# Kernel optimization log

Hardware: AMD Instinct MI355X
Metric: run time of the kernel (lower is better)

Reference implementation:

```python
import jax, jax.numpy as jnp
import numpy as np

HC = 4           # hc_mult
ITERS = 20       # hc_sinkhorn_iters
EPS = 1e-6       # hc_eps
NORM_EPS = 1e-6  # rms_norm_eps


def setup_inputs() -> dict:
    key = jax.random.key(0)
    k = jax.random.split(key, 4)
    B, S, H = 1, 4096, 4096
    mix = (2 + HC) * HC  # 24
    hidden_states = jax.random.normal(k[0], (B, S, HC, H), jnp.float32)
    hc_fn = jax.random.normal(k[1], (mix, HC * H), jnp.float32) * 0.02
    hc_base = jax.random.normal(k[2], (mix,), jnp.float32) * 0.02
    hc_scale = jnp.ones((3,), jnp.float32)
    norm_weight = jnp.ones((H,), jnp.float32)
    w_inner = jax.random.normal(k[3], (H, H), jnp.float32) * 0.02
    return {
        "hidden_states": hidden_states,
        "hc_fn": hc_fn,
        "hc_base": hc_base,
        "hc_scale": hc_scale,
        "norm_weight": norm_weight,
        "w_inner": w_inner,
    }


def reference(hidden_states, hc_fn, hc_base, hc_scale, norm_weight, w_inner):
    B, S, hc, H = hidden_states.shape
    # RMS stat over the flattened (hc*H) feature dim
    flat = hidden_states.reshape(B, S, hc * H).astype(jnp.float32)
    rs = jax.lax.rsqrt(jnp.mean(jnp.square(flat), axis=-1, keepdims=True) + NORM_EPS)
    mixes = jnp.einsum('bsd,md->bsm', flat, hc_fn) * rs  # [B,S,(2+hc)*hc]

    ps, qs, cs = hc_scale[0], hc_scale[1], hc_scale[2]
    pre = jax.nn.sigmoid(mixes[..., :hc] * ps + hc_base[:hc]) + EPS           # [B,S,hc]
    post = jax.nn.sigmoid(mixes[..., hc:2 * hc] * qs + hc_base[hc:2 * hc]) + EPS
    comb = jax.nn.sigmoid(
        mixes[..., 2 * hc:].reshape(B, S, hc, hc) * cs
        + hc_base[2 * hc:].reshape(hc, hc)
    ) + EPS  # [B,S,hc,hc]

    # 20-iter Sinkhorn row/column normalization
    def sink(_, c):
        c = c / (jnp.sum(c, axis=-1, keepdims=True) + EPS)
        return c / (jnp.sum(c, axis=-2, keepdims=True) + EPS)
    comb = jax.lax.fori_loop(0, ITERS, sink, comb)

    # weighted stream reduction -> [B,S,H]
    reduced = jnp.einsum('bsh,bshd->bsd', pre, hidden_states)

    # norm + inner sub-block (RMSNorm then dense projection)
    nr = jax.lax.rsqrt(jnp.mean(jnp.square(reduced), axis=-1, keepdims=True) + NORM_EPS)
    normed = reduced * nr * norm_weight
    out = jnp.einsum('bsd,ed->bse', normed, w_inner)  # [B,S,H]

    # broadcast back to streams: post-gated write + Sinkhorn-mixed residual
    expanded = post[..., None] * out[:, :, None, :] \
        + jnp.einsum('bshk,bskd->bshd', comb, hidden_states)
    return expanded.astype(hidden_states.dtype)
```

## Files before the change

kernel.cpp:

```cpp
#include <hip/hip_runtime.h>
#include <math.h>

#define S_DIM 4096
#define H_DIM 4096
#define HC_N 4
#define HD_DIM 16384
#define MIXN 24
#define SINK_IT 20

typedef float f32x4 __attribute__((ext_vector_type(4)));
typedef __bf16 bf16x8 __attribute__((ext_vector_type(8)));
typedef unsigned short u16x8 __attribute__((ext_vector_type(8)));
typedef unsigned short u16x4 __attribute__((ext_vector_type(4)));

__device__ __forceinline__ unsigned short f2bf(float f) {
  unsigned u = __builtin_bit_cast(unsigned, f);
  u += 0x7FFFu + ((u >> 16) & 1u);
  return (unsigned short)(u >> 16);
}
__device__ __forceinline__ float bf2f(unsigned short h) {
  return __builtin_bit_cast(float, (unsigned)h << 16);
}

__global__ __launch_bounds__(256) void k_w2bf(const float* __restrict__ w,
                                              unsigned short* __restrict__ wb) {
  const size_t i = (size_t)(blockIdx.x * 256 + threadIdx.x) * 8;
  f32x4 a = *(const f32x4*)(w + i);
  f32x4 b = *(const f32x4*)(w + i + 4);
  u16x8 o;
  o[0] = f2bf(a.x); o[1] = f2bf(a.y); o[2] = f2bf(a.z); o[3] = f2bf(a.w);
  o[4] = f2bf(b.x); o[5] = f2bf(b.y); o[6] = f2bf(b.z); o[7] = f2bf(b.w);
  *(u16x8*)(wb + i) = o;
}

__global__ __launch_bounds__(256) void k_mixes(const float* __restrict__ hs,
                                               const float* __restrict__ fn,
                                               float* __restrict__ mixraw,
                                               float* __restrict__ sumsq) {
  __shared__ __align__(16) float lds[HC_N][1024];
  const int tid = threadIdx.x;
  const int b = blockIdx.x;
  const int lane = tid & 63, wave = tid >> 6;
  const int mbase = wave * 6;

  float acc[HC_N][6];
  float ss[HC_N];
#pragma unroll
  for (int r = 0; r < HC_N; r++) {
    ss[r] = 0.f;
#pragma unroll
    for (int j = 0; j < 6; j++) acc[r][j] = 0.f;
  }

  const size_t rowbase = (size_t)b * HC_N * HD_DIM;
  for (int it = 0; it < 16; ++it) {
    __syncthreads();
#pragma unroll
    for (int r = 0; r < HC_N; r++) {
      f32x4 v = *(const f32x4*)(hs + rowbase + (size_t)r * HD_DIM + it * 1024 + tid * 4);
      *(f32x4*)(&lds[r][tid * 4]) = v;
    }
    __syncthreads();
#pragma unroll
    for (int ii = 0; ii < 4; ii++) {
      const int c4 = ii * 64 + lane;
      f32x4 h4[HC_N];
#pragma unroll
      for (int r = 0; r < HC_N; r++) h4[r] = *(const f32x4*)(&lds[r][c4 * 4]);
      if (wave == 0) {
#pragma unroll
        for (int r = 0; r < HC_N; r++)
          ss[r] += h4[r].x * h4[r].x + h4[r].y * h4[r].y + h4[r].z * h4[r].z + h4[r].w * h4[r].w;
      }
#pragma unroll
      for (int j = 0; j < 6; j++) {
        f32x4 fv = *(const f32x4*)(fn + (size_t)(mbase + j) * HD_DIM + it * 1024 + c4 * 4);
#pragma unroll
        for (int r = 0; r < HC_N; r++)
          acc[r][j] += h4[r].x * fv.x + h4[r].y * fv.y + h4[r].z * fv.z + h4[r].w * fv.w;
      }
    }
  }

#pragma unroll
  for (int r = 0; r < HC_N; r++) {
#pragma unroll
    for (int j = 0; j < 6; j++) {
      float v = acc[r][j];
#pragma unroll
      for (int off = 32; off >= 1; off >>= 1) v += __shfl_xor(v, off, 64);
      if (lane == 0) mixraw[(size_t)(b * 4 + r) * MIXN + mbase + j] = v;
    }
  }
  if (wave == 0) {
#pragma unroll
    for (int r = 0; r < HC_N; r++) {
      float v = ss[r];
#pragma unroll
      for (int off = 32; off >= 1; off >>= 1) v += __shfl_xor(v, off, 64);
      if (lane == 0) sumsq[b * 4 + r] = v;
    }
  }
}

__global__ __launch_bounds__(256) void k_gates(const float* __restrict__ mixraw,
                                               const float* __restrict__ sumsq,
                                               const float* __restrict__ hbase,
                                               const float* __restrict__ hscale,
                                               float* __restrict__ gates) {
  const int row = blockIdx.x * 256 + threadIdx.x;
  const float rs = rsqrtf(sumsq[row] * (1.0f / HD_DIM) + 1e-6f);
  const float ps = hscale[0], qs = hscale[1], cs = hscale[2];
  const float* mr = mixraw + (size_t)row * MIXN;
  float g[MIXN];
#pragma unroll
  for (int m = 0; m < MIXN; m++) {
    const float sc = (m < 4) ? ps : ((m < 8) ? qs : cs);
    const float x = mr[m] * rs * sc + hbase[m];
    g[m] = 1.0f / (1.0f + expf(-x)) + 1e-6f;
  }
  for (int t = 0; t < SINK_IT; t++) {
#pragma unroll
    for (int i = 0; i < 4; i++) {
      const float s = g[8 + i * 4 + 0] + g[8 + i * 4 + 1] + g[8 + i * 4 + 2] + g[8 + i * 4 + 3] + 1e-6f;
#pragma unroll
      for (int j = 0; j < 4; j++) g[8 + i * 4 + j] /= s;
    }
#pragma unroll
    for (int j = 0; j < 4; j++) {
      const float s = g[8 + 0 + j] + g[8 + 4 + j] + g[8 + 8 + j] + g[8 + 12 + j] + 1e-6f;
#pragma unroll
      for (int i = 0; i < 4; i++) g[8 + i * 4 + j] /= s;
    }
  }
  float* go = gates + (size_t)row * MIXN;
#pragma unroll
  for (int m = 0; m < MIXN; m++) go[m] = g[m];
}

__global__ __launch_bounds__(256) void k_reduce_norm(const float* __restrict__ hs,
                                                     const float* __restrict__ gates,
                                                     const float* __restrict__ nw,
                                                     unsigned short* __restrict__ normed) {
  const int s = blockIdx.x, tid = threadIdx.x;
  const int lane = tid & 63, wave = tid >> 6;
  const float* g = gates + (size_t)s * MIXN;
  const float p0 = g[0], p1 = g[1], p2 = g[2], p3 = g[3];
  const size_t base = (size_t)s * HC_N * H_DIM;

  f32x4 red[4];
  float ssq = 0.f;
#pragma unroll
  for (int it = 0; it < 4; ++it) {
    const int d4 = it * 256 + tid;
    f32x4 a = *(const f32x4*)(hs + base + (size_t)0 * H_DIM + (size_t)d4 * 4);
    f32x4 b = *(const f32x4*)(hs + base + (size_t)1 * H_DIM + (size_t)d4 * 4);
    f32x4 c = *(const f32x4*)(hs + base + (size_t)2 * H_DIM + (size_t)d4 * 4);
    f32x4 d = *(const f32x4*)(hs + base + (size_t)3 * H_DIM + (size_t)d4 * 4);
    f32x4 v = p0 * a + p1 * b + p2 * c + p3 * d;
    red[it] = v;
    ssq += v.x * v.x + v.y * v.y + v.z * v.z + v.w * v.w;
  }
#pragma unroll
  for (int off = 32; off >= 1; off >>= 1) ssq += __shfl_xor(ssq, off, 64);
  __shared__ float ls[4];
  if (lane == 0) ls[wave] = ssq;
  __syncthreads();
  const float tot = ls[0] + ls[1] + ls[2] + ls[3];
  const float nr = rsqrtf(tot * (1.0f / H_DIM) + 1e-6f);
#pragma unroll
  for (int it = 0; it < 4; ++it) {
    const int d4 = it * 256 + tid;
    f32x4 w = *(const f32x4*)(nw + (size_t)d4 * 4);
    f32x4 v = red[it] * nr;
    v = v * w;
    u16x4 o;
    o[0] = f2bf(v.x); o[1] = f2bf(v.y); o[2] = f2bf(v.z); o[3] = f2bf(v.w);
    *(u16x4*)(normed + (size_t)s * H_DIM + (size_t)d4 * 4) = o;
  }
}

__device__ __forceinline__ void gload_lds16(const unsigned short* g, unsigned short* l) {
  __builtin_amdgcn_global_load_lds(
      (const __attribute__((address_space(1))) unsigned int*)(const void*)g,
      (__attribute__((address_space(3))) unsigned int*)(void*)l, 16, 0, 0);
}

#define VMW(n) asm volatile("s_waitcnt vmcnt(" #n ")" ::: "memory")
#define BAR    asm volatile("s_barrier" ::: "memory")
#define LGK0   asm volatile("s_waitcnt lgkmcnt(0)" ::: "memory")
#define SCB    __builtin_amdgcn_sched_barrier(0)

__global__ __launch_bounds__(512, 2) void k_gemm(const unsigned short* __restrict__ A,
                                                 const unsigned short* __restrict__ B,
                                                 unsigned short* __restrict__ C) {
  __shared__ __align__(16) unsigned short sAbuf[2][2][256 * 32];
  __shared__ __align__(16) unsigned short sBbuf[2][2][256 * 32];
  const int tid = threadIdx.x;
  const int lane = tid & 63, wave = tid >> 6;

  const int bid = blockIdx.x;
  const int v = bid & 7, u = bid >> 3;
  const int bm = u & 15, bn = v * 2 + (u >> 4);
  const int wm = wave >> 2, wn = wave & 3;

  const int srow = lane >> 2;
  const int sk8 = (((lane & 3) ^ ((lane >> 3) & 3)) * 8);
  const unsigned short* gA = A + (size_t)(bm * 256 + wave * 32 + srow) * 4096 + sk8;
  const unsigned short* gB = B + (size_t)(bn * 256 + wave * 32 + srow) * 4096 + sk8;
  const int ld0 = wave * 1024 + lane * 8;
  const int ld1 = ld0 + 512;

  f32x4 acc[8][4];
  f32x4 zero = {0.f, 0.f, 0.f, 0.f};
#pragma unroll
  for (int mf = 0; mf < 8; mf++)
#pragma unroll
    for (int nf = 0; nf < 4; nf++) acc[mf][nf] = zero;
  bf16x8 af[8];

  const int frow = lane & 15;
  const int fk = (((lane >> 4) ^ ((lane >> 1) & 3)) * 8);

#define PHASE_BODY(db, kh, nh, dostg, sdst, gsrc, t, skh) do {                  \
    if ((nh) == 0) {                                                            \
      _Pragma("unroll") for (int mf = 0; mf < 8; mf++)                          \
        af[mf] = *(const bf16x8*)&sAbuf[db][kh][(wm * 128 + mf * 16 + frow) * 32 + fk]; \
    }                                                                           \
    bf16x8 b0 = *(const bf16x8*)&sBbuf[db][kh][(wn * 64 + ((nh) * 2 + 0) * 16 + frow) * 32 + fk]; \
    bf16x8 b1 = *(const bf16x8*)&sBbuf[db][kh][(wn * 64 + ((nh) * 2 + 1) * 16 + frow) * 32 + fk]; \
    if (dostg) {                                                                \
      const unsigned short* _g = (gsrc) + (size_t)(t) * 64 + (skh) * 32;        \
      gload_lds16(_g,              (sdst) + ld0);                               \
      gload_lds16(_g + 16 * 4096,  (sdst) + ld1);                               \
    }                                                                           \
    SCB;                                                                        \
    BAR;                                                                        \
    LGK0;                                                                       \
    SCB;                                                                        \
    __builtin_amdgcn_s_setprio(1);                                              \
    _Pragma("unroll") for (int mf = 0; mf < 8; mf++) {                          \
      acc[mf][(nh) * 2 + 0] = __builtin_amdgcn_mfma_f32_16x16x32_bf16(af[mf], b0, acc[mf][(nh) * 2 + 0], 0, 0, 0); \
      acc[mf][(nh) * 2 + 1] = __builtin_amdgcn_mfma_f32_16x16x32_bf16(af[mf], b1, acc[mf][(nh) * 2 + 1], 0, 0, 0); \
    }                                                                           \
    __builtin_amdgcn_s_setprio(0);                                              \
    SCB;                                                                        \
  } while (0)

  gload_lds16(gA,                  &sAbuf[0][0][0] + ld0);
  gload_lds16(gA + 16 * 4096,      &sAbuf[0][0][0] + ld1);
  gload_lds16(gB,                  &sBbuf[0][0][0] + ld0);
  gload_lds16(gB + 16 * 4096,      &sBbuf[0][0][0] + ld1);
  gload_lds16(gA + 32,             &sAbuf[0][1][0] + ld0);
  gload_lds16(gA + 32 + 16 * 4096, &sAbuf[0][1][0] + ld1);
  gload_lds16(gB + 32,             &sBbuf[0][1][0] + ld0);
  gload_lds16(gB + 32 + 16 * 4096, &sBbuf[0][1][0] + ld1);
  VMW(4);
  BAR;

  for (int i = 0; i < 31; ++i) {
    const int t1 = 2 * i + 1, t2 = 2 * i + 2;
    PHASE_BODY(0, 0, 0, 1, &sAbuf[1][0][0], gA, t1, 0);          BAR;
    PHASE_BODY(0, 0, 1, 1, &sBbuf[1][0][0], gB, t1, 0); VMW(4);  BAR;
    PHASE_BODY(0, 1, 0, 1, &sAbuf[1][1][0], gA, t1, 1);          BAR;
    PHASE_BODY(0, 1, 1, 1, &sBbuf[1][1][0], gB, t1, 1); VMW(4);  BAR;
    PHASE_BODY(1, 0, 0, 1, &sAbuf[0][0][0], gA, t2, 0);          BAR;
    PHASE_BODY(1, 0, 1, 1, &sBbuf[0][0][0], gB, t2, 0); VMW(4);  BAR;
    PHASE_BODY(1, 1, 0, 1, &sAbuf[0][1][0], gA, t2, 1);          BAR;
    PHASE_BODY(1, 1, 1, 1, &sBbuf[0][1][0], gB, t2, 1); VMW(4);  BAR;
  }
  PHASE_BODY(0, 0, 0, 1, &sAbuf[1][0][0], gA, 63, 0);            BAR;
  PHASE_BODY(0, 0, 1, 1, &sBbuf[1][0][0], gB, 63, 0); VMW(4);    BAR;
  PHASE_BODY(0, 1, 0, 1, &sAbuf[1][1][0], gA, 63, 1);            BAR;
  PHASE_BODY(0, 1, 1, 1, &sBbuf[1][1][0], gB, 63, 1); VMW(0);    BAR;
  PHASE_BODY(1, 0, 0, 0, &sAbuf[0][0][0], gA, 0, 0);             BAR;
  PHASE_BODY(1, 0, 1, 0, &sAbuf[0][0][0], gA, 0, 0);             BAR;
  PHASE_BODY(1, 1, 0, 0, &sAbuf[0][0][0], gA, 0, 0);             BAR;
  PHASE_BODY(1, 1, 1, 0, &sAbuf[0][0][0], gA, 0, 0);

#undef PHASE_BODY

  const int crow0 = bm * 256 + wm * 128 + (lane >> 4) * 4;
  const int ccol0 = bn * 256 + wn * 64 + (lane & 15);
#pragma unroll
  for (int mf = 0; mf < 8; mf++)
#pragma unroll
    for (int nf = 0; nf < 4; nf++)
#pragma unroll
      for (int j = 0; j < 4; j++)
        C[(size_t)(crow0 + mf * 16 + j) * 4096 + ccol0 + nf * 16] = f2bf(acc[mf][nf][j]);
}

__global__ __launch_bounds__(256) void k_expand(const float* __restrict__ hs,
                                                const unsigned short* __restrict__ outb,
                                                const float* __restrict__ gates,
                                                float* __restrict__ y) {
  const int s = blockIdx.x, tid = threadIdx.x;
  const float* g = gates + (size_t)s * MIXN;
  float post[4], cb[4][4];
#pragma unroll
  for (int h = 0; h < 4; h++) post[h] = g[4 + h];
#pragma unroll
  for (int h = 0; h < 4; h++)
#pragma unroll
    for (int k = 0; k < 4; k++) cb[h][k] = g[8 + h * 4 + k];

  const size_t base = (size_t)s * HC_N * H_DIM;
#pragma unroll
  for (int it = 0; it < 4; ++it) {
    const int d4 = it * 256 + tid;
    f32x4 hv[4];
#pragma unroll
    for (int k = 0; k < 4; k++)
      hv[k] = *(const f32x4*)(hs + base + (size_t)k * H_DIM + (size_t)d4 * 4);
    u16x4 ob = *(const u16x4*)(outb + (size_t)s * H_DIM + (size_t)d4 * 4);
    f32x4 o = {bf2f(ob[0]), bf2f(ob[1]), bf2f(ob[2]), bf2f(ob[3])};
#pragma unroll
    for (int h = 0; h < 4; h++) {
      f32x4 e = post[h] * o + cb[h][0] * hv[0] + cb[h][1] * hv[1] + cb[h][2] * hv[2] + cb[h][3] * hv[3];
      *(f32x4*)(y + base + (size_t)h * H_DIM + (size_t)d4 * 4) = e;
    }
  }
}

extern "C" void kernel_launch(void* const* d_in, const int* in_sizes, int n_in,
                              void* d_out, int out_size, void* d_ws, size_t ws_size,
                              hipStream_t stream) {
  const float* hs = (const float*)d_in[0];
  const float* fn = (const float*)d_in[1];
  const float* hbase = (const float*)d_in[2];
  const float* hscale = (const float*)d_in[3];
  const float* nw = (const float*)d_in[4];
  const float* wi = (const float*)d_in[5];
  float* y = (float*)d_out;

  char* ws = (char*)d_ws;
  float* mixraw = (float*)(ws);
  float* sumsq = (float*)(ws + 393216);
  float* gates = (float*)(ws + 409600);
  unsigned short* normed = (unsigned short*)(ws + 1048576);
  unsigned short* wb = (unsigned short*)(ws + 1048576 + 33554432);
  unsigned short* outb = (unsigned short*)(ws + 1048576 + 2 * 33554432);

  k_w2bf<<<8192, 256, 0, stream>>>(wi, wb);
  k_mixes<<<1024, 256, 0, stream>>>(hs, fn, mixraw, sumsq);
  k_gates<<<16, 256, 0, stream>>>(mixraw, sumsq, hbase, hscale, gates);
  k_reduce_norm<<<4096, 256, 0, stream>>>(hs, gates, nw, normed);
  k_gemm<<<256, 512, 0, stream>>>(normed, wb, outb);
  k_expand<<<4096, 256, 0, stream>>>(hs, outb, gates, y);
}
```

Baseline: 484.3 us.

## Fuse gate/Sinkhorn computation into mixes kernel and register-prefetch inputs

Merges the separate gates kernel into the mixes kernel, so per-row mix results and sum-of-squares stay in shared memory and the gates are written directly. The mixes loop drops the LDS staging and block barriers: each wave now loads hidden-state and hc_fn vectors straight from global memory, with a one-iteration register prefetch. This removes one launch and the round trip of the intermediate buffers. The cost is that all four waves now read the same hidden-state data redundantly from global memory or cache, and the Sinkhorn tail runs on only four threads per block.

```diff
diff --git a/kernel.cpp b/kernel.cpp
--- a/kernel.cpp
+++ b/kernel.cpp
@@ -35,107 +35,110 @@
 
 __global__ __launch_bounds__(256) void k_mixes(const float* __restrict__ hs,
                                                const float* __restrict__ fn,
-                                               float* __restrict__ mixraw,
-                                               float* __restrict__ sumsq) {
-  __shared__ __align__(16) float lds[HC_N][1024];
-  const int tid = threadIdx.x;
-  const int b = blockIdx.x;
-  const int lane = tid & 63, wave = tid >> 6;
-  const int mbase = wave * 6;
-
-  float acc[HC_N][6];
-  float ss[HC_N];
-#pragma unroll
-  for (int r = 0; r < HC_N; r++) {
-    ss[r] = 0.f;
-#pragma unroll
-    for (int j = 0; j < 6; j++) acc[r][j] = 0.f;
-  }
-
-  const size_t rowbase = (size_t)b * HC_N * HD_DIM;
-  for (int it = 0; it < 16; ++it) {
-    __syncthreads();
-#pragma unroll
-    for (int r = 0; r < HC_N; r++) {
-      f32x4 v = *(const f32x4*)(hs + rowbase + (size_t)r * HD_DIM + it * 1024 + tid * 4);
-      *(f32x4*)(&lds[r][tid * 4]) = v;
-    }
-    __syncthreads();
-#pragma unroll
-    for (int ii = 0; ii < 4; ii++) {
-      const int c4 = ii * 64 + lane;
-      f32x4 h4[HC_N];
-#pragma unroll
-      for (int r = 0; r < HC_N; r++) h4[r] = *(const f32x4*)(&lds[r][c4 * 4]);
-      if (wave == 0) {
-#pragma unroll
-        for (int r = 0; r < HC_N; r++)
-          ss[r] += h4[r].x * h4[r].x + h4[r].y * h4[r].y + h4[r].z * h4[r].z + h4[r].w * h4[r].w;
-      }
-#pragma unroll
-      for (int j = 0; j < 6; j++) {
-        f32x4 fv = *(const f32x4*)(fn + (size_t)(mbase + j) * HD_DIM + it * 1024 + c4 * 4);
-#pragma unroll
-        for (int r = 0; r < HC_N; r++)
-          acc[r][j] += h4[r].x * fv.x + h4[r].y * fv.y + h4[r].z * fv.z + h4[r].w * fv.w;
-      }
-    }
-  }
-
-#pragma unroll
-  for (int r = 0; r < HC_N; r++) {
-#pragma unroll
-    for (int j = 0; j < 6; j++) {
-      float v = acc[r][j];
-#pragma unroll
-      for (int off = 32; off >= 1; off >>= 1) v += __shfl_xor(v, off, 64);
-      if (lane == 0) mixraw[(size_t)(b * 4 + r) * MIXN + mbase + j] = v;
-    }
-  }
-  if (wave == 0) {
-#pragma unroll
-    for (int r = 0; r < HC_N; r++) {
-      float v = ss[r];
-#pragma unroll
-      for (int off = 32; off >= 1; off >>= 1) v += __shfl_xor(v, off, 64);
-      if (lane == 0) sumsq[b * 4 + r] = v;
-    }
-  }
-}
-
-__global__ __launch_bounds__(256) void k_gates(const float* __restrict__ mixraw,
-                                               const float* __restrict__ sumsq,
                                                const float* __restrict__ hbase,
                                                const float* __restrict__ hscale,
                                                float* __restrict__ gates) {
-  const int row = blockIdx.x * 256 + threadIdx.x;
-  const float rs = rsqrtf(sumsq[row] * (1.0f / HD_DIM) + 1e-6f);
-  const float ps = hscale[0], qs = hscale[1], cs = hscale[2];
-  const float* mr = mixraw + (size_t)row * MIXN;
-  float g[MIXN];
-#pragma unroll
-  for (int m = 0; m < MIXN; m++) {
-    const float sc = (m < 4) ? ps : ((m < 8) ? qs : cs);
-    const float x = mr[m] * rs * sc + hbase[m];
-    g[m] = 1.0f / (1.0f + expf(-x)) + 1e-6f;
-  }
-  for (int t = 0; t < SINK_IT; t++) {
-#pragma unroll
-    for (int i = 0; i < 4; i++) {
-      const float s = g[8 + i * 4 + 0] + g[8 + i * 4 + 1] + g[8 + i * 4 + 2] + g[8 + i * 4 + 3] + 1e-6f;
-#pragma unroll
-      for (int j = 0; j < 4; j++) g[8 + i * 4 + j] /= s;
-    }
-#pragma unroll
-    for (int j = 0; j < 4; j++) {
-      const float s = g[8 + 0 + j] + g[8 + 4 + j] + g[8 + 8 + j] + g[8 + 12 + j] + 1e-6f;
-#pragma unroll
-      for (int i = 0; i < 4; i++) g[8 + i * 4 + j] /= s;
-    }
-  }
-  float* go = gates + (size_t)row * MIXN;
-#pragma unroll
-  for (int m = 0; m < MIXN; m++) go[m] = g[m];
+  __shared__ float smix[HC_N][MIXN];
+  __shared__ float sss[HC_N];
+  const int tid = threadIdx.x, lane = tid & 63, wave = tid >> 6;
+  const int mb = wave * 6;
+  const size_t rowbase = (size_t)blockIdx.x * HC_N * HD_DIM;
+  const float* fb = fn + (size_t)mb * HD_DIM;
+
+  float acc[HC_N][6];
+#pragma unroll
+  for (int r = 0; r < HC_N; r++)
+#pragma unroll
+    for (int j = 0; j < 6; j++) acc[r][j] = 0.f;
+  float ss[HC_N] = {0.f, 0.f, 0.f, 0.f};
+
+  f32x4 ph[HC_N], pf[6];
+  {
+    const int d0 = lane * 4;
+#pragma unroll
+    for (int r = 0; r < HC_N; r++)
+      ph[r] = *(const f32x4*)(hs + rowbase + (size_t)r * HD_DIM + d0);
+#pragma unroll
+    for (int j = 0; j < 6; j++)
+      pf[j] = *(const f32x4*)(fb + (size_t)j * HD_DIM + d0);
+  }
+
+  for (int it = 0; it < 64; ++it) {
+    f32x4 h4[HC_N], fv[6];
+#pragma unroll
+    for (int r = 0; r < HC_N; r++) h4[r] = ph[r];
+#pragma unroll
+    for (int j = 0; j < 6; j++) fv[j] = pf[j];
+    if (it + 1 < 64) {
+      const int dn = ((it + 1) * 64 + lane) * 4;
+#pragma unroll
+      for (int r = 0; r < HC_N; r++)
+        ph[r] = *(const f32x4*)(hs + rowbase + (size_t)r * HD_DIM + dn);
+#pragma unroll
+      for (int j = 0; j < 6; j++)
+        pf[j] = *(const f32x4*)(fb + (size_t)j * HD_DIM + dn);
+    }
+    if (wave == 0) {
+#pragma unroll
+      for (int r = 0; r < HC_N; r++)
+        ss[r] += h4[r].x * h4[r].x + h4[r].y * h4[r].y + h4[r].z * h4[r].z + h4[r].w * h4[r].w;
+    }
+#pragma unroll
+    for (int j = 0; j < 6; j++)
+#pragma unroll
+      for (int r = 0; r < HC_N; r++)
+        acc[r][j] += h4[r].x * fv[j].x + h4[r].y * fv[j].y + h4[r].z * fv[j].z + h4[r].w * fv[j].w;
+  }
+
+#pragma unroll
+  for (int r = 0; r < HC_N; r++)
+#pragma unroll
+    for (int j = 0; j < 6; j++) {
+      float v = acc[r][j];
+#pragma unroll
+      for (int off = 32; off >= 1; off >>= 1) v += __shfl_xor(v, off, 64);
+      if (lane == 0) smix[r][mb + j] = v;
+    }
+  if (wave == 0) {
+#pragma unroll
+    for (int r = 0; r < HC_N; r++) {
+      float v = ss[r];
+#pragma unroll
+      for (int off = 32; off >= 1; off >>= 1) v += __shfl_xor(v, off, 64);
+      if (lane == 0) sss[r] = v;
+    }
+  }
+  __syncthreads();
+
+  if (tid < HC_N) {
+    const int r = tid;
+    const float rs = rsqrtf(sss[r] * (1.0f / HD_DIM) + 1e-6f);
+    const float ps = hscale[0], qs = hscale[1], cs = hscale[2];
+    float g[MIXN];
+#pragma unroll
+    for (int m = 0; m < MIXN; m++) {
+      const float sc = (m < 4) ? ps : ((m < 8) ? qs : cs);
+      const float x = smix[r][m] * rs * sc + hbase[m];
+      g[m] = 1.0f / (1.0f + expf(-x)) + 1e-6f;
+    }
+    for (int t = 0; t < SINK_IT; t++) {
+#pragma unroll
+      for (int i = 0; i < 4; i++) {
+        const float s = g[8 + i * 4 + 0] + g[8 + i * 4 + 1] + g[8 + i * 4 + 2] + g[8 + i * 4 + 3] + 1e-6f;
+#pragma unroll
+        for (int j = 0; j < 4; j++) g[8 + i * 4 + j] /= s;
+      }
+#pragma unroll
+      for (int j = 0; j < 4; j++) {
+        const float s = g[8 + 0 + j] + g[8 + 4 + j] + g[8 + 8 + j] + g[8 + 12 + j] + 1e-6f;
+#pragma unroll
+        for (int i = 0; i < 4; i++) g[8 + i * 4 + j] /= s;
+      }
+    }
+    float* go = gates + (size_t)(blockIdx.x * HC_N + r) * MIXN;
+#pragma unroll
+    for (int m = 0; m < MIXN; m++) go[m] = g[m];
+  }
 }
 
 __global__ __launch_bounds__(256) void k_reduce_norm(const float* __restrict__ hs,
@@ -335,16 +338,13 @@
   float* y = (float*)d_out;
 
   char* ws = (char*)d_ws;
-  float* mixraw = (float*)(ws);
-  float* sumsq = (float*)(ws + 393216);
   float* gates = (float*)(ws + 409600);
   unsigned short* normed = (unsigned short*)(ws + 1048576);
   unsigned short* wb = (unsigned short*)(ws + 1048576 + 33554432);
   unsigned short* outb = (unsigned short*)(ws + 1048576 + 2 * 33554432);
 
   k_w2bf<<<8192, 256, 0, stream>>>(wi, wb);
-  k_mixes<<<1024, 256, 0, stream>>>(hs, fn, mixraw, sumsq);
-  k_gates<<<16, 256, 0, stream>>>(mixraw, sumsq, hbase, hscale, gates);
+  k_mixes<<<1024, 256, 0, stream>>>(hs, fn, hbase, hscale, gates);
   k_reduce_norm<<<4096, 256, 0, stream>>>(hs, gates, nw, normed);
   k_gemm<<<256, 512, 0, stream>>>(normed, wb, outb);
   k_expand<<<4096, 256, 0, stream>>>(hs, outb, gates, y);
```

Result: slower. 506.8 us (+4.6%).
